# Kernel optimization log

Measured on AMD Instinct MI355X. Metric: run time of the kernel, lower is better.

## Reference

```python
import jax, jax.numpy as jnp
import numpy as np

N, E, D, H, OUT = 100000, 1600000, 64, 64, 4


def _glorot(key, i, o):
    s = (6.0 / (i + o)) ** 0.5
    return jax.random.uniform(key, (i, o), jnp.float32, -s, s)


def setup_inputs() -> dict:
    key = jax.random.key(0)
    ks = jax.random.split(key, 5)
    x = jax.random.normal(ks[0], (N, D), jnp.float32)
    edge_index = jax.random.randint(ks[1], (2, E), 0, N, jnp.int32)
    return {
        "x": x,
        "edge_index": edge_index,
        "W0": _glorot(ks[2], D, H), "b0": jnp.zeros((H,), jnp.float32),
        "W1": _glorot(ks[3], H, H), "b1": jnp.zeros((H,), jnp.float32),
        "W2": _glorot(ks[4], H, OUT), "b2": jnp.zeros((OUT,), jnp.float32),
    }


def _gcn_layer(x, src, dst, W, b):
    # WeightedGCNConv.forward: remove_self_loops, then gcn_norm with
    # add_self_loops=True (self-loop weight 1), symmetric normalization,
    # scatter-add aggregation, then Linear.
    n = x.shape[0]
    w = (src != dst).astype(x.dtype)           # zero out original self loops
    deg = jax.ops.segment_sum(w, dst, num_segments=n) + 1.0  # +1 from added self loop
    dis = jax.lax.rsqrt(deg)                   # deg >= 1, no inf
    norm = dis[src] * w * dis[dst]             # [E]
    agg = jax.ops.segment_sum(norm[:, None] * x[src], dst, num_segments=n)
    agg = agg + (dis * dis)[:, None] * x       # self-loop contribution
    return agg @ W + b


def reference(x, edge_index, W0, b0, W1, b1, W2, b2):
    src, dst = edge_index[0], edge_index[1]    # flow source_to_target
    # Dropout is identity in eval mode.
    h = jax.nn.relu(_gcn_layer(x, src, dst, W0, b0))
    h = jax.nn.relu(_gcn_layer(h, src, dst, W1, b1))
    return _gcn_layer(h, src, dst, W2, b2)     # [N, 4]
```

## Files before the change

kernel.cpp:

```cpp
#include <hip/hip_runtime.h>
#include <hip/hip_fp16.h>


#define BLK 256
#define NBITS 7
#define NBW   (1 << NBITS)
#define G     8
#define CHUNK 4096
#define EPT   (CHUNK / BLK)
#define CAPG  384
#define PAD   16

__global__ void k_zero_i(int* __restrict__ p, int n) {
    int i = blockIdx.x * blockDim.x + threadIdx.x;
    if (i < n) p[i] = 0;
}

__global__ void k_binA(const int* __restrict__ src, const int* __restrict__ dst,
                       int* __restrict__ bcur, int* __restrict__ binned,
                       int E, int nb) {
    __shared__ int lcnt[1024];
    __shared__ int lbase[1024];
    int t = threadIdx.x;
    int g = blockIdx.x & (G - 1);
    for (int i = t; i < nb; i += BLK) lcnt[i] = 0;
    __syncthreads();

    int e0 = blockIdx.x * CHUNK;
    int bs[EPT], vs[EPT];
#pragma unroll
    for (int i = 0; i < EPT; ++i) {
        int e = e0 + i * BLK + t;
        bs[i] = -1;
        if (e < E) {
            int s = src[e], d = dst[e];
            if (s != d) {
                bs[i] = d >> NBITS;
                vs[i] = (s << NBITS) | (d & (NBW - 1));
                atomicAdd(&lcnt[bs[i]], 1);
            }
        }
    }
    __syncthreads();
    for (int i = t; i < nb; i += BLK) {
        int c = lcnt[i];
        lbase[i] = c ? atomicAdd(&bcur[(g * nb + i) * PAD], c) : 0;
    }
    __syncthreads();
    for (int i = t; i < nb; i += BLK) lcnt[i] = 0;
    __syncthreads();
#pragma unroll
    for (int i = 0; i < EPT; ++i) {
        if (bs[i] >= 0) {
            int p = lbase[bs[i]] + atomicAdd(&lcnt[bs[i]], 1);
            if (p < CAPG) binned[(size_t)(g * nb + bs[i]) * CAPG + p] = vs[i];
        }
    }
}

__global__ void k_bscan(const int* __restrict__ bcur, int* __restrict__ bbase, int nb) {
    __shared__ int sh[1024];
    int t = threadIdx.x;
    int v = 0;
    if (t < nb)
        for (int g = 0; g < G; ++g) v += min(bcur[(g * nb + t) * PAD], CAPG);
    sh[t] = v;
    __syncthreads();
    for (int off = 1; off < 1024; off <<= 1) {
        int u = (t >= off) ? sh[t - off] : 0;
        __syncthreads();
        sh[t] += u;
        __syncthreads();
    }
    if (t < nb) bbase[t] = sh[t] - v;
}

__global__ void k_binB(const int* __restrict__ bcur, const int* __restrict__ binned,
                       const int* __restrict__ bbase, int* __restrict__ rowstart,
                       float* __restrict__ dis, int* __restrict__ srcs,
                       int n, int nb) {
    __shared__ int cnt[NBW];
    __shared__ int scan[NBW];
    int b = blockIdx.x;
    int t = threadIdx.x;
    if (t < NBW) cnt[t] = 0;
    __syncthreads();
    for (int g = 0; g < G; ++g) {
        int m = min(bcur[(g * nb + b) * PAD], CAPG);
        const int* reg = binned + (size_t)(g * nb + b) * CAPG;
        for (int i = t; i < m; i += BLK)
            atomicAdd(&cnt[reg[i] & (NBW - 1)], 1);
    }
    __syncthreads();
    int c = 0;
    if (t < NBW) { c = cnt[t]; scan[t] = c; }
    __syncthreads();
    for (int off = 1; off < NBW; off <<= 1) {
        int u = (t < NBW && t >= off) ? scan[t - off] : 0;
        __syncthreads();
        if (t < NBW) scan[t] += u;
        __syncthreads();
    }
    int base = bbase[b];
    if (t < NBW) {
        int excl = scan[t] - c;
        int node = b * NBW + t;
        if (node < n) {
            rowstart[node] = base + excl;
            dis[node] = rsqrtf((float)c + 1.0f);
        }
        if (node == n) rowstart[n] = base + excl;
    }
    __syncthreads();
    if (t < NBW) scan[t] = scan[t] - c;
    __syncthreads();
    for (int g = 0; g < G; ++g) {
        int m = min(bcur[(g * nb + b) * PAD], CAPG);
        const int* reg = binned + (size_t)(g * nb + b) * CAPG;
        for (int i = t; i < m; i += BLK) {
            int v = reg[i];
            int p = atomicAdd(&scan[v & (NBW - 1)], 1);
            srcs[base + p] = v >> NBITS;
        }
    }
}

__device__ __forceinline__ float ldf(const float* p, long i) { return p[i]; }
__device__ __forceinline__ float ldf(const __half* p, long i) { return __half2float(p[i]); }

template <bool RELU, typename TIN>
__global__ void k_gemm64(const TIN* __restrict__ in, const float* __restrict__ W,
                         const float* __restrict__ dis, __half* __restrict__ z16, int n) {
    __shared__ float rows[4][64];
    int c  = threadIdx.x & 63;
    int r4 = threadIdx.x >> 6;
    float Wr[64];
#pragma unroll
    for (int k = 0; k < 64; ++k) Wr[k] = W[k * 64 + c];
    const float4* rp = reinterpret_cast<const float4*>(&rows[r4][0]);
    for (long base = (long)blockIdx.x * 4; base < n; base += (long)gridDim.x * 4) {
        long row = base + r4;
        __syncthreads();
        if (row < n) {
            float v = ldf(in, row * 64 + c);
            rows[r4][c] = RELU ? fmaxf(v, 0.0f) : v;
        }
        __syncthreads();
        if (row < n) {
            float acc = 0.0f;
#pragma unroll
            for (int k4 = 0; k4 < 16; ++k4) {
                float4 rv = rp[k4];
                acc = fmaf(rv.x, Wr[4 * k4 + 0], acc);
                acc = fmaf(rv.y, Wr[4 * k4 + 1], acc);
                acc = fmaf(rv.z, Wr[4 * k4 + 2], acc);
                acc = fmaf(rv.w, Wr[4 * k4 + 3], acc);
            }
            z16[row * 64 + c] = __float2half(dis[row] * acc);
        }
    }
}

template <bool FUSEW2>
__global__ void k_aggregate(const float2* __restrict__ zrow, const int* __restrict__ rowstart,
                            const int* __restrict__ srcs, const float* __restrict__ dis,
                            const float* __restrict__ bias, const float* __restrict__ W2,
                            uint2* __restrict__ agg, float* __restrict__ y2, int n) {
    __shared__ float W2l[64 * 4];
    if constexpr (FUSEW2) {
        if (threadIdx.x < 256) W2l[threadIdx.x] = W2[threadIdx.x];
        __syncthreads();
    }
    int lane = threadIdx.x & 63;
    int node = blockIdx.x * (BLK / 64) + (threadIdx.x >> 6);
    if (node >= n) return;
    int p  = lane & 15;
    int hi = lane >> 4;
    float4 acc = make_float4(0.f, 0.f, 0.f, 0.f);
    if (hi == 0) {
        float2 r = zrow[(long)node * 16 + p];
        float2 a = __half22float2(*reinterpret_cast<__half2*>(&r.x));
        float2 bq = __half22float2(*reinterpret_cast<__half2*>(&r.y));
        acc = make_float4(a.x, a.y, bq.x, bq.y);
    }
    int beg = rowstart[node], end = rowstart[node + 1];
    for (int base = beg; base < end; base += 64) {
        int m = min(end - base, 64);
        int s = (lane < m) ? srcs[base + lane] : 0;
        int mf = m & ~3;
#pragma unroll 8
        for (int j = 0; j < mf; j += 4) {
            int sj = __shfl(s, j + hi);
            float2 r = zrow[(long)sj * 16 + p];
            float2 a = __half22float2(*reinterpret_cast<__half2*>(&r.x));
            float2 bq = __half22float2(*reinterpret_cast<__half2*>(&r.y));
            acc.x += a.x; acc.y += a.y; acc.z += bq.x; acc.w += bq.y;
        }
        if (m & 3) {
            int idx = mf + hi;
            int sj = __shfl(s, idx < 64 ? idx : 63);
            if (idx < m) {
                float2 r = zrow[(long)sj * 16 + p];
                float2 a = __half22float2(*reinterpret_cast<__half2*>(&r.x));
                float2 bq = __half22float2(*reinterpret_cast<__half2*>(&r.y));
                acc.x += a.x; acc.y += a.y; acc.z += bq.x; acc.w += bq.y;
            }
        }
    }
    acc.x += __shfl_xor(acc.x, 16); acc.y += __shfl_xor(acc.y, 16);
    acc.z += __shfl_xor(acc.z, 16); acc.w += __shfl_xor(acc.w, 16);
    acc.x += __shfl_xor(acc.x, 32); acc.y += __shfl_xor(acc.y, 32);
    acc.z += __shfl_xor(acc.z, 32); acc.w += __shfl_xor(acc.w, 32);

    float dd = dis[node];
    float4 bb = reinterpret_cast<const float4*>(bias)[p];
    if constexpr (!FUSEW2) {
        if (hi == 0) {
            __half2 o0 = __floats2half2_rn(dd * acc.x + bb.x, dd * acc.y + bb.y);
            __half2 o1 = __floats2half2_rn(dd * acc.z + bb.z, dd * acc.w + bb.w);
            uint2 u;
            u.x = *reinterpret_cast<unsigned int*>(&o0);
            u.y = *reinterpret_cast<unsigned int*>(&o1);
            agg[(long)node * 16 + p] = u;
        }
    } else {
        float h0 = fmaxf(dd * acc.x + bb.x, 0.f);
        float h1 = fmaxf(dd * acc.y + bb.y, 0.f);
        float h2 = fmaxf(dd * acc.z + bb.z, 0.f);
        float h3 = fmaxf(dd * acc.w + bb.w, 0.f);
        float pc[4];
#pragma unroll
        for (int c = 0; c < 4; ++c) {
            pc[c] = h0 * W2l[(4 * p + 0) * 4 + c] + h1 * W2l[(4 * p + 1) * 4 + c]
                  + h2 * W2l[(4 * p + 2) * 4 + c] + h3 * W2l[(4 * p + 3) * 4 + c];
        }
#pragma unroll
        for (int off = 1; off < 16; off <<= 1) {
#pragma unroll
            for (int c = 0; c < 4; ++c) pc[c] += __shfl_xor(pc[c], off);
        }
        if (lane == 0) {
            reinterpret_cast<float4*>(y2)[node] =
                make_float4(dd * pc[0], dd * pc[1], dd * pc[2], dd * pc[3]);
        }
    }
}

__global__ void k_agg4(const float* __restrict__ z2, const int* __restrict__ rowstart,
                       const int* __restrict__ srcs, const float* __restrict__ dis,
                       const float* __restrict__ b, float* __restrict__ out, int n) {
    long t = (long)blockIdx.x * blockDim.x + threadIdx.x;
    int i = (int)(t >> 2), c = (int)(t & 3);
    if (i < n) {
        float acc = z2[(long)i * 4 + c];
        int beg = rowstart[i], end = rowstart[i + 1];
        for (int e = beg; e < end; ++e)
            acc += z2[(long)srcs[e] * 4 + c];
        out[(long)i * 4 + c] = dis[i] * acc + b[c];
    }
}

extern "C" void kernel_launch(void* const* d_in, const int* in_sizes, int n_in,
                              void* d_out, int out_size, void* d_ws, size_t ws_size,
                              hipStream_t stream) {
    const float* x  = (const float*)d_in[0];
    const int*   ei = (const int*)d_in[1];
    const float* W0 = (const float*)d_in[2];
    const float* b0 = (const float*)d_in[3];
    const float* W1 = (const float*)d_in[4];
    const float* b1 = (const float*)d_in[5];
    const float* W2 = (const float*)d_in[6];
    const float* b2 = (const float*)d_in[7];
    float* out = (float*)d_out;

    const int n = in_sizes[0] / 64;
    const int E = in_sizes[1] / 2;
    const int* src = ei;
    const int* dst = ei + E;
    const int nb = (n + NBW - 1) / NBW;

    int*    bcur     = (int*)d_ws;
    int*    bbase    = bcur + G * nb * PAD;
    int*    rowstart = bbase + nb + 1;
    int*    srcs     = rowstart + n + 1;
    float*  dis      = (float*)(srcs + E);
    __half* z16      = (__half*)(dis + n);
    __half* bufA     = z16 + (size_t)n * 64;
    float*  y2       = (float*)(bufA + (size_t)n * 64);
    int*    binned   = (int*)bufA;

    const int gWave  = (n + (BLK / 64) - 1) / (BLK / 64);
    const int gN4    = (int)(((long)n * 4 + BLK - 1) / BLK);
    const int gGemm  = 2048;
    const int nchunk = (E + CHUNK - 1) / CHUNK;

    k_zero_i<<<(G * nb * PAD + BLK - 1) / BLK, BLK, 0, stream>>>(bcur, G * nb * PAD);
    k_binA<<<nchunk, BLK, 0, stream>>>(src, dst, bcur, binned, E, nb);
    k_bscan<<<1, 1024, 0, stream>>>(bcur, bbase, nb);
    k_binB<<<nb, BLK, 0, stream>>>(bcur, binned, bbase, rowstart, dis, srcs, n, nb);

    k_gemm64<false, float><<<gGemm, BLK, 0, stream>>>(x, W0, dis, z16, n);
    k_aggregate<false><<<gWave, BLK, 0, stream>>>((const float2*)z16, rowstart, srcs, dis,
                                                  b0, nullptr, (uint2*)bufA, nullptr, n);

    k_gemm64<true, __half><<<gGemm, BLK, 0, stream>>>(bufA, W1, dis, z16, n);
    k_aggregate<true><<<gWave, BLK, 0, stream>>>((const float2*)z16, rowstart, srcs, dis,
                                                 b1, W2, nullptr, y2, n);

    k_agg4<<<gN4, BLK, 0, stream>>>(y2, rowstart, srcs, dis, b2, out, n);
}
```

Measured before the change: 256.5 us.

## Fuse layer-1 aggregation with W1 GEMM and replace zero kernel with memset

The first aggregation kernel now applies bias and ReLU, stages each node's hidden row in shared memory, and multiplies it by W1 in the same wave. The resulting scaled fp16 z1 feeds the second aggregation directly. This removes one kernel launch and an intermediate fp16 write and re-read of the N×64 hidden activations. The cost is that every wave now loads all of W1 into 64 registers per node, which adds register pressure and may lower occupancy in the gather kernel. A custom zeroing kernel is also swapped for hipMemsetAsync.

```diff
diff --git a/kernel.cpp b/kernel.cpp
--- a/kernel.cpp
+++ b/kernel.cpp
@@ -10,11 +10,6 @@
 #define EPT   (CHUNK / BLK)
 #define CAPG  384
 #define PAD   16
-
-__global__ void k_zero_i(int* __restrict__ p, int n) {
-    int i = blockIdx.x * blockDim.x + threadIdx.x;
-    if (i < n) p[i] = 0;
-}
 
 __global__ void k_binA(const int* __restrict__ src, const int* __restrict__ dst,
                        int* __restrict__ bcur, int* __restrict__ binned,
@@ -125,11 +120,7 @@
     }
 }
 
-__device__ __forceinline__ float ldf(const float* p, long i) { return p[i]; }
-__device__ __forceinline__ float ldf(const __half* p, long i) { return __half2float(p[i]); }
-
-template <bool RELU, typename TIN>
-__global__ void k_gemm64(const TIN* __restrict__ in, const float* __restrict__ W,
+__global__ void k_gemm64(const float* __restrict__ in, const float* __restrict__ W,
                          const float* __restrict__ dis, __half* __restrict__ z16, int n) {
     __shared__ float rows[4][64];
     int c  = threadIdx.x & 63;
@@ -141,10 +132,7 @@
     for (long base = (long)blockIdx.x * 4; base < n; base += (long)gridDim.x * 4) {
         long row = base + r4;
         __syncthreads();
-        if (row < n) {
-            float v = ldf(in, row * 64 + c);
-            rows[r4][c] = RELU ? fmaxf(v, 0.0f) : v;
-        }
+        if (row < n) rows[r4][c] = in[row * 64 + c];
         __syncthreads();
         if (row < n) {
             float acc = 0.0f;
@@ -161,21 +149,10 @@
     }
 }
 
-template <bool FUSEW2>
-__global__ void k_aggregate(const float2* __restrict__ zrow, const int* __restrict__ rowstart,
-                            const int* __restrict__ srcs, const float* __restrict__ dis,
-                            const float* __restrict__ bias, const float* __restrict__ W2,
-                            uint2* __restrict__ agg, float* __restrict__ y2, int n) {
-    __shared__ float W2l[64 * 4];
-    if constexpr (FUSEW2) {
-        if (threadIdx.x < 256) W2l[threadIdx.x] = W2[threadIdx.x];
-        __syncthreads();
-    }
-    int lane = threadIdx.x & 63;
-    int node = blockIdx.x * (BLK / 64) + (threadIdx.x >> 6);
-    if (node >= n) return;
-    int p  = lane & 15;
-    int hi = lane >> 4;
+__device__ __forceinline__ float4 gather_row(const float2* __restrict__ zrow,
+                                             const int* __restrict__ rowstart,
+                                             const int* __restrict__ srcs,
+                                             int node, int lane, int p, int hi) {
     float4 acc = make_float4(0.f, 0.f, 0.f, 0.f);
     if (hi == 0) {
         float2 r = zrow[(long)node * 16 + p];
@@ -211,38 +188,84 @@
     acc.z += __shfl_xor(acc.z, 16); acc.w += __shfl_xor(acc.w, 16);
     acc.x += __shfl_xor(acc.x, 32); acc.y += __shfl_xor(acc.y, 32);
     acc.z += __shfl_xor(acc.z, 32); acc.w += __shfl_xor(acc.w, 32);
+    return acc;
+}
+
+__global__ void k_aggW1(const float2* __restrict__ zrow, const int* __restrict__ rowstart,
+                        const int* __restrict__ srcs, const float* __restrict__ dis,
+                        const float* __restrict__ b0, const float* __restrict__ W1,
+                        __half* __restrict__ z1, int n) {
+    __shared__ float hrow[4][64];
+    int lane = threadIdx.x & 63;
+    int wv   = threadIdx.x >> 6;
+    int node = blockIdx.x * (BLK / 64) + wv;
+    if (node >= n) return;
+    int p = lane & 15, hi = lane >> 4;
+
+    float4 acc = gather_row(zrow, rowstart, srcs, node, lane, p, hi);
 
     float dd = dis[node];
-    float4 bb = reinterpret_cast<const float4*>(bias)[p];
-    if constexpr (!FUSEW2) {
-        if (hi == 0) {
-            __half2 o0 = __floats2half2_rn(dd * acc.x + bb.x, dd * acc.y + bb.y);
-            __half2 o1 = __floats2half2_rn(dd * acc.z + bb.z, dd * acc.w + bb.w);
-            uint2 u;
-            u.x = *reinterpret_cast<unsigned int*>(&o0);
-            u.y = *reinterpret_cast<unsigned int*>(&o1);
-            agg[(long)node * 16 + p] = u;
-        }
-    } else {
-        float h0 = fmaxf(dd * acc.x + bb.x, 0.f);
-        float h1 = fmaxf(dd * acc.y + bb.y, 0.f);
-        float h2 = fmaxf(dd * acc.z + bb.z, 0.f);
-        float h3 = fmaxf(dd * acc.w + bb.w, 0.f);
-        float pc[4];
-#pragma unroll
-        for (int c = 0; c < 4; ++c) {
-            pc[c] = h0 * W2l[(4 * p + 0) * 4 + c] + h1 * W2l[(4 * p + 1) * 4 + c]
-                  + h2 * W2l[(4 * p + 2) * 4 + c] + h3 * W2l[(4 * p + 3) * 4 + c];
-        }
-#pragma unroll
-        for (int off = 1; off < 16; off <<= 1) {
-#pragma unroll
-            for (int c = 0; c < 4; ++c) pc[c] += __shfl_xor(pc[c], off);
-        }
-        if (lane == 0) {
-            reinterpret_cast<float4*>(y2)[node] =
-                make_float4(dd * pc[0], dd * pc[1], dd * pc[2], dd * pc[3]);
-        }
+    float4 bb = reinterpret_cast<const float4*>(b0)[p];
+    if (hi == 0) {
+        float4 h;
+        h.x = fmaxf(dd * acc.x + bb.x, 0.f);
+        h.y = fmaxf(dd * acc.y + bb.y, 0.f);
+        h.z = fmaxf(dd * acc.z + bb.z, 0.f);
+        h.w = fmaxf(dd * acc.w + bb.w, 0.f);
+        *reinterpret_cast<float4*>(&hrow[wv][4 * p]) = h;
+    }
+    asm volatile("s_waitcnt lgkmcnt(0)" ::: "memory");
+
+    float Wr[64];
+#pragma unroll
+    for (int k = 0; k < 64; ++k) Wr[k] = W1[k * 64 + lane];
+    const float4* hq = reinterpret_cast<const float4*>(&hrow[wv][0]);
+    float o = 0.f;
+#pragma unroll
+    for (int k4 = 0; k4 < 16; ++k4) {
+        float4 hv = hq[k4];
+        o = fmaf(hv.x, Wr[4 * k4 + 0], o);
+        o = fmaf(hv.y, Wr[4 * k4 + 1], o);
+        o = fmaf(hv.z, Wr[4 * k4 + 2], o);
+        o = fmaf(hv.w, Wr[4 * k4 + 3], o);
+    }
+    z1[(long)node * 64 + lane] = __float2half(dd * o);
+}
+
+__global__ void k_aggW2(const float2* __restrict__ zrow, const int* __restrict__ rowstart,
+                        const int* __restrict__ srcs, const float* __restrict__ dis,
+                        const float* __restrict__ b1, const float* __restrict__ W2,
+                        float* __restrict__ y2, int n) {
+    __shared__ float W2l[64 * 4];
+    if (threadIdx.x < 256) W2l[threadIdx.x] = W2[threadIdx.x];
+    __syncthreads();
+    int lane = threadIdx.x & 63;
+    int node = blockIdx.x * (BLK / 64) + (threadIdx.x >> 6);
+    if (node >= n) return;
+    int p = lane & 15, hi = lane >> 4;
+
+    float4 acc = gather_row(zrow, rowstart, srcs, node, lane, p, hi);
+
+    float dd = dis[node];
+    float4 bb = reinterpret_cast<const float4*>(b1)[p];
+    float h0 = fmaxf(dd * acc.x + bb.x, 0.f);
+    float h1 = fmaxf(dd * acc.y + bb.y, 0.f);
+    float h2 = fmaxf(dd * acc.z + bb.z, 0.f);
+    float h3 = fmaxf(dd * acc.w + bb.w, 0.f);
+    float pc[4];
+#pragma unroll
+    for (int c = 0; c < 4; ++c) {
+        pc[c] = h0 * W2l[(4 * p + 0) * 4 + c] + h1 * W2l[(4 * p + 1) * 4 + c]
+              + h2 * W2l[(4 * p + 2) * 4 + c] + h3 * W2l[(4 * p + 3) * 4 + c];
+    }
+#pragma unroll
+    for (int off = 1; off < 16; off <<= 1) {
+#pragma unroll
+        for (int c = 0; c < 4; ++c) pc[c] += __shfl_xor(pc[c], off);
+    }
+    if (lane == 0) {
+        reinterpret_cast<float4*>(y2)[node] =
+            make_float4(dd * pc[0], dd * pc[1], dd * pc[2], dd * pc[3]);
     }
 }
 
@@ -285,27 +308,27 @@
     int*    srcs     = rowstart + n + 1;
     float*  dis      = (float*)(srcs + E);
     __half* z16      = (__half*)(dis + n);
-    __half* bufA     = z16 + (size_t)n * 64;
-    float*  y2       = (float*)(bufA + (size_t)n * 64);
-    int*    binned   = (int*)bufA;
+    __half* z1       = z16 + (size_t)n * 64;
+    float*  y2       = (float*)(z1 + (size_t)n * 64);
+    int*    binned   = (int*)z1;
 
     const int gWave  = (n + (BLK / 64) - 1) / (BLK / 64);
     const int gN4    = (int)(((long)n * 4 + BLK - 1) / BLK);
     const int gGemm  = 2048;
     const int nchunk = (E + CHUNK - 1) / CHUNK;
 
-    k_zero_i<<<(G * nb * PAD + BLK - 1) / BLK, BLK, 0, stream>>>(bcur, G * nb * PAD);
+    hipMemsetAsync(bcur, 0, (size_t)G * nb * PAD * sizeof(int), stream);
     k_binA<<<nchunk, BLK, 0, stream>>>(src, dst, bcur, binned, E, nb);
     k_bscan<<<1, 1024, 0, stream>>>(bcur, bbase, nb);
     k_binB<<<nb, BLK, 0, stream>>>(bcur, binned, bbase, rowstart, dis, srcs, n, nb);
 
-    k_gemm64<false, float><<<gGemm, BLK, 0, stream>>>(x, W0, dis, z16, n);
-    k_aggregate<false><<<gWave, BLK, 0, stream>>>((const float2*)z16, rowstart, srcs, dis,
-                                                  b0, nullptr, (uint2*)bufA, nullptr, n);
-
-    k_gemm64<true, __half><<<gGemm, BLK, 0, stream>>>(bufA, W1, dis, z16, n);
-    k_aggregate<true><<<gWave, BLK, 0, stream>>>((const float2*)z16, rowstart, srcs, dis,
-                                                 b1, W2, nullptr, y2, n);
+    k_gemm64<<<gGemm, BLK, 0, stream>>>(x, W0, dis, z16, n);
+
+    k_aggW1<<<gWave, BLK, 0, stream>>>((const float2*)z16, rowstart, srcs, dis, b0, W1,
+                                       z1, n);
+
+    k_aggW2<<<gWave, BLK, 0, stream>>>((const float2*)z1, rowstart, srcs, dis, b1, W2,
+                                       y2, n);
 
     k_agg4<<<gN4, BLK, 0, stream>>>(y2, rowstart, srcs, dis, b2, out, n);
 }
```

Measured after the change: 252.2 us. Within noise of the previous version (-1.7%).
